# Optimization experiments

Hardware: AMD Instinct MI355X
Metric: run time of the kernel (lower is better)

The kernel has to match this reference:

```python
import jax, jax.numpy as jnp
import numpy as np

B, S, K, V = 2048, 128, 128, 128  # S == K == V required by the original code's matmul/broadcast
W_MAX = 1.0


def setup_inputs() -> dict:
    key = jax.random.key(0)
    ks = jax.random.split(key, 10)
    sc = 0.05
    return {
        "obs": jax.random.normal(ks[0], (B, S, K), jnp.float32),
        "brim_hidden": jax.random.normal(ks[1], (B, S, V), jnp.float32),
        "modulation": jax.random.uniform(ks[2], (B, S, 1), jnp.float32),
        "w_assoc": jax.random.normal(ks[3], (B, K, V), jnp.float32) * 0.1,
        "key_W": jax.random.normal(ks[4], (K, K), jnp.float32) * sc,
        "key_b": jnp.zeros((K,), jnp.float32),
        "val_W": jax.random.normal(ks[5], (V, V), jnp.float32) * sc,
        "val_b": jnp.zeros((V,), jnp.float32),
        "A_w": jax.random.normal(ks[6], (K, V), jnp.float32) * sc,
        "B_w": jax.random.normal(ks[7], (K, V), jnp.float32) * sc,
        "done_process_mdp": jnp.ones((B,), jnp.int32),
    }


def reference(obs, brim_hidden, modulation, w_assoc, key_W, key_b, val_W, val_b, A_w, B_w, done_process_mdp):
    # Encoders: single Linear each (key_encoder_layer = value_encoder_layer = 0)
    k = jnp.einsum("bsk,ok->bso", obs, key_W) + key_b            # [B,S,K]
    v = jnp.einsum("bsv,ov->bso", brim_hidden, val_W) + val_b    # [B,S,V]
    v = modulation * v                                           # neuromodulated values
    # Hebbian correlation and self-regularization terms
    corr = jnp.einsum("bsk,bsv->bkv", k, v)                      # key^T @ value  [B,K,V]
    reg = jnp.matmul(k, k)                                       # literal matmul(key, key); S==K -> [B,K,K]==[B,K,V]
    # Decay-scaled elementwise combine (A_w/B_w broadcast over batch)
    delta_w = A_w * (W_MAX - w_assoc) * corr - B_w * w_assoc * reg
    # Scatter update at done indices (mask form, equivalent since indices are unique)
    done = done_process_mdp.astype(bool)[:, None, None]
    return jnp.where(done, w_assoc + delta_w, w_assoc)
```

## Files before the change

### kernel.cpp

```cpp
#include <hip/hip_runtime.h>


typedef __attribute__((ext_vector_type(8))) short bf16x8;
typedef __attribute__((ext_vector_type(4))) float f32x4;

constexpr int D   = 128;
constexpr int LDB = 136;

__device__ __forceinline__ short f2bf(float x) {
    unsigned u = __builtin_bit_cast(unsigned, x);
    u += 0x7fff + ((u >> 16) & 1);
    return (short)(u >> 16);
}

__global__ void cvt_weights(const float* __restrict__ kw,
                            const float* __restrict__ vw,
                            short* __restrict__ o) {
    int i = blockIdx.x * 256 + threadIdx.x;
    o[i]         = f2bf(kw[i]);
    o[16384 + i] = f2bf(vw[i]);
}

__global__ __launch_bounds__(512, 1)
void hebb_mfma(const float* __restrict__ obs,
               const float* __restrict__ brim,
               const float* __restrict__ modu,
               const float* __restrict__ was,
               const short* __restrict__ keyWb,
               const float* __restrict__ keyB,
               const short* __restrict__ valWb,
               const float* __restrict__ valB,
               const float* __restrict__ Aw,
               const float* __restrict__ Bw,
               const int* __restrict__ done,
               float* __restrict__ out)
{
    __shared__ __align__(16) short xS [D * LDB];
    __shared__ __align__(16) short kS [D * LDB];
    __shared__ __align__(16) short kTS[D * LDB];
    __shared__ __align__(16) short vTS[D * LDB];

    const int b  = blockIdx.x;
    const int t  = threadIdx.x;
    const int w  = t >> 6;
    const int l  = t & 63;
    const int lr = l & 15;
    const int hg = l >> 4;

    {
        const float4* src = (const float4*)(obs + (size_t)b * D * D);
        #pragma unroll
        for (int i = 0; i < 8; ++i) {
            float4 g = src[i * 512 + t];
            int f = (i * 512 + t) * 4;
            int row = f >> 7, col = f & 127;
            short4 s4 = make_short4(f2bf(g.x), f2bf(g.y), f2bf(g.z), f2bf(g.w));
            *(short4*)&xS[row * LDB + col] = s4;
        }
    }
    __syncthreads();

    f32x4 acc[8], acc2[8];
    #pragma unroll
    for (int i = 0; i < 8; ++i) { acc[i] = f32x4{0.f,0.f,0.f,0.f}; acc2[i] = f32x4{0.f,0.f,0.f,0.f}; }

    for (int c = 0; c < 4; ++c) {
        const int c0 = c * 32 + 8 * hg;
        bf16x8 aK = *(const bf16x8*)&xS[(16 * w + lr) * LDB + c0];
        bf16x8 aT = *(const bf16x8*)&keyWb[(16 * w + lr) * D + c0];
        #pragma unroll
        for (int q = 0; q < 8; ++q) {
            bf16x8 bK = *(const bf16x8*)&keyWb[(16 * q + lr) * D + c0];
            bf16x8 bT = *(const bf16x8*)&xS[(16 * q + lr) * LDB + c0];
            acc[q]  = __builtin_amdgcn_mfma_f32_16x16x32_bf16(aK, bK, acc[q],  0, 0, 0);
            acc2[q] = __builtin_amdgcn_mfma_f32_16x16x32_bf16(aT, bT, acc2[q], 0, 0, 0);
        }
    }
    {
        float kbR[4];
        #pragma unroll
        for (int r = 0; r < 4; ++r) kbR[r] = keyB[16 * w + 4 * hg + r];
        #pragma unroll
        for (int q = 0; q < 8; ++q) {
            float kbC = keyB[16 * q + lr];
            #pragma unroll
            for (int r = 0; r < 4; ++r) {
                kS [(16 * w + 4 * hg + r) * LDB + 16 * q + lr] = f2bf(acc[q][r]  + kbC);
                kTS[(16 * w + 4 * hg + r) * LDB + 16 * q + lr] = f2bf(acc2[q][r] + kbR[r]);
            }
        }
    }
    __syncthreads();

    {
        const float4* src = (const float4*)(brim + (size_t)b * D * D);
        #pragma unroll
        for (int i = 0; i < 8; ++i) {
            float4 g = src[i * 512 + t];
            int f = (i * 512 + t) * 4;
            int row = f >> 7, col = f & 127;
            short4 s4 = make_short4(f2bf(g.x), f2bf(g.y), f2bf(g.z), f2bf(g.w));
            *(short4*)&xS[row * LDB + col] = s4;
        }
    }
    __syncthreads();

    #pragma unroll
    for (int i = 0; i < 8; ++i) acc[i] = f32x4{0.f,0.f,0.f,0.f};
    for (int c = 0; c < 4; ++c) {
        const int c0 = c * 32 + 8 * hg;
        bf16x8 aV = *(const bf16x8*)&valWb[(16 * w + lr) * D + c0];
        #pragma unroll
        for (int q = 0; q < 8; ++q) {
            bf16x8 bV = *(const bf16x8*)&xS[(16 * q + lr) * LDB + c0];
            acc[q] = __builtin_amdgcn_mfma_f32_16x16x32_bf16(aV, bV, acc[q], 0, 0, 0);
        }
    }
    {
        float vbR[4];
        #pragma unroll
        for (int r = 0; r < 4; ++r) vbR[r] = valB[16 * w + 4 * hg + r];
        #pragma unroll
        for (int q = 0; q < 8; ++q) {
            float m = modu[(size_t)b * D + 16 * q + lr];
            #pragma unroll
            for (int r = 0; r < 4; ++r)
                vTS[(16 * w + 4 * hg + r) * LDB + 16 * q + lr] = f2bf(m * (acc[q][r] + vbR[r]));
        }
    }
    __syncthreads();

    f32x4 cacc[8], racc[8];
    #pragma unroll
    for (int i = 0; i < 8; ++i) { cacc[i] = f32x4{0.f,0.f,0.f,0.f}; racc[i] = f32x4{0.f,0.f,0.f,0.f}; }

    for (int c = 0; c < 4; ++c) {
        const int c0 = c * 32 + 8 * hg;
        bf16x8 aC = *(const bf16x8*)&kTS[(16 * w + lr) * LDB + c0];
        bf16x8 aR = *(const bf16x8*)&kS [(16 * w + lr) * LDB + c0];
        #pragma unroll
        for (int q = 0; q < 8; ++q) {
            bf16x8 bC = *(const bf16x8*)&vTS[(16 * q + lr) * LDB + c0];
            bf16x8 bR = *(const bf16x8*)&kTS[(16 * q + lr) * LDB + c0];
            cacc[q] = __builtin_amdgcn_mfma_f32_16x16x32_bf16(aC, bC, cacc[q], 0, 0, 0);
            racc[q] = __builtin_amdgcn_mfma_f32_16x16x32_bf16(aR, bR, racc[q], 0, 0, 0);
        }
    }

    const float dsc = done[b] ? 1.0f : 0.0f;
    const size_t ob = (size_t)b * D * D;
    #pragma unroll
    for (int q = 0; q < 8; ++q) {
        const int j = 16 * q + lr;
        #pragma unroll
        for (int r = 0; r < 4; ++r) {
            const int i  = 16 * w + 4 * hg + r;
            const int ij = i * D + j;
            float wv = was[ob + ij];
            out[ob + ij] = wv + dsc * (Aw[ij] * (1.0f - wv) * cacc[q][r]
                                     - Bw[ij] * wv * racc[q][r]);
        }
    }
}

extern "C" void kernel_launch(void* const* d_in, const int* in_sizes, int n_in,
                              void* d_out, int out_size, void* d_ws, size_t ws_size,
                              hipStream_t stream) {
    const float* obs  = (const float*)d_in[0];
    const float* brim = (const float*)d_in[1];
    const float* modu = (const float*)d_in[2];
    const float* was  = (const float*)d_in[3];
    const float* keyW = (const float*)d_in[4];
    const float* keyB = (const float*)d_in[5];
    const float* valW = (const float*)d_in[6];
    const float* valB = (const float*)d_in[7];
    const float* Aw   = (const float*)d_in[8];
    const float* Bw   = (const float*)d_in[9];
    const int*   done = (const int*)d_in[10];
    float* out = (float*)d_out;

    const int B = in_sizes[10];
    short* wb = (short*)d_ws;

    hipLaunchKernelGGL(cvt_weights, dim3(64), dim3(256), 0, stream, keyW, valW, wb);
    hipLaunchKernelGGL(hebb_mfma, dim3(B), dim3(512), 0, stream,
                       obs, brim, modu, was, wb, keyB, wb + 16384, valB,
                       Aw, Bw, done, out);
}
```

Measured before the change: 494.9 us.

## Process eight batches per block with register prefetch and coalesced epilogue

Makes each workgroup loop over eight batch elements, so the grid is B/8 blocks. The next batch's obs and brim tiles and the current w_assoc tile are loaded into registers ahead of time, so global loads overlap with MFMA work. The epilogue stages corr and reg through LDS as bf16, which allows coalesced float4 reads of w_assoc, Aw and Bw and coalesced float4 writes of the output. Barriers become a lightweight lgkmcnt wait plus s_barrier. The costs are extra bf16 rounding of corr and reg, higher register pressure, and only 256 blocks, which may underfill the GPU.

```diff
diff --git a/kernel.cpp b/kernel.cpp
--- a/kernel.cpp
+++ b/kernel.cpp
@@ -6,12 +6,21 @@
 
 constexpr int D   = 128;
 constexpr int LDB = 136;
+constexpr int LDC = 132;
+constexpr int BPB = 8;
 
 __device__ __forceinline__ short f2bf(float x) {
     unsigned u = __builtin_bit_cast(unsigned, x);
     u += 0x7fff + ((u >> 16) & 1);
     return (short)(u >> 16);
 }
+__device__ __forceinline__ float bf2f(short s) {
+    unsigned u = ((unsigned)(unsigned short)s) << 16;
+    return __builtin_bit_cast(float, u);
+}
+
+#define LBAR() do { asm volatile("s_waitcnt lgkmcnt(0)" ::: "memory"); \
+                    __builtin_amdgcn_s_barrier(); } while (0)
 
 __global__ void cvt_weights(const float* __restrict__ kw,
                             const float* __restrict__ vw,
@@ -40,126 +49,168 @@
     __shared__ __align__(16) short kTS[D * LDB];
     __shared__ __align__(16) short vTS[D * LDB];
 
-    const int b  = blockIdx.x;
     const int t  = threadIdx.x;
     const int w  = t >> 6;
     const int l  = t & 63;
     const int lr = l & 15;
     const int hg = l >> 4;
-
+    const int b0 = blockIdx.x * BPB;
+
+    float kbR[4], vbR[4], kbC[8], vbC[8];
+    #pragma unroll
+    for (int r = 0; r < 4; ++r) { kbR[r] = keyB[16*w + 4*hg + r]; vbR[r] = valB[16*w + 4*hg + r]; }
+    #pragma unroll
+    for (int q = 0; q < 8; ++q) { kbC[q] = keyB[16*q + lr]; vbC[q] = valB[16*q + lr]; }
+    (void)vbC;
+
+    float4 obsR[8], brimR[8], wasR[8];
     {
-        const float4* src = (const float4*)(obs + (size_t)b * D * D);
+        const float4* os = (const float4*)(obs  + (size_t)b0 * D * D);
+        const float4* bs = (const float4*)(brim + (size_t)b0 * D * D);
+        #pragma unroll
+        for (int i = 0; i < 8; ++i) { obsR[i] = os[i*512 + t]; brimR[i] = bs[i*512 + t]; }
+    }
+    #pragma unroll
+    for (int i = 0; i < 8; ++i) {
+        int f = (i * 512 + t) * 4;
+        int row = f >> 7, col = f & 127;
+        *(short4*)&xS[row * LDB + col] =
+            make_short4(f2bf(obsR[i].x), f2bf(obsR[i].y), f2bf(obsR[i].z), f2bf(obsR[i].w));
+    }
+    LBAR();
+
+    for (int it = 0; it < BPB; ++it) {
+        const int b  = b0 + it;
+        const size_t ob = (size_t)b * D * D;
+
+        f32x4 acc[8], acc2[8];
+        #pragma unroll
+        for (int i = 0; i < 8; ++i) { acc[i] = f32x4{0.f,0.f,0.f,0.f}; acc2[i] = f32x4{0.f,0.f,0.f,0.f}; }
+
+        for (int c = 0; c < 4; ++c) {
+            const int c0 = c * 32 + 8 * hg;
+            bf16x8 aK = *(const bf16x8*)&xS[(16*w + lr) * LDB + c0];
+            bf16x8 aT = *(const bf16x8*)&keyWb[(16*w + lr) * D + c0];
+            #pragma unroll
+            for (int q = 0; q < 8; ++q) {
+                bf16x8 bK = *(const bf16x8*)&keyWb[(16*q + lr) * D + c0];
+                bf16x8 bT = *(const bf16x8*)&xS[(16*q + lr) * LDB + c0];
+                acc[q]  = __builtin_amdgcn_mfma_f32_16x16x32_bf16(aK, bK, acc[q],  0, 0, 0);
+                acc2[q] = __builtin_amdgcn_mfma_f32_16x16x32_bf16(aT, bT, acc2[q], 0, 0, 0);
+            }
+        }
+        #pragma unroll
+        for (int q = 0; q < 8; ++q) {
+            #pragma unroll
+            for (int r = 0; r < 4; ++r) {
+                kS [(16*w + 4*hg + r) * LDB + 16*q + lr] = f2bf(acc[q][r]  + kbC[q]);
+                kTS[(16*w + 4*hg + r) * LDB + 16*q + lr] = f2bf(acc2[q][r] + kbR[r]);
+            }
+        }
+        LBAR();
+
         #pragma unroll
         for (int i = 0; i < 8; ++i) {
-            float4 g = src[i * 512 + t];
             int f = (i * 512 + t) * 4;
             int row = f >> 7, col = f & 127;
-            short4 s4 = make_short4(f2bf(g.x), f2bf(g.y), f2bf(g.z), f2bf(g.w));
-            *(short4*)&xS[row * LDB + col] = s4;
-        }
-    }
-    __syncthreads();
-
-    f32x4 acc[8], acc2[8];
-    #pragma unroll
-    for (int i = 0; i < 8; ++i) { acc[i] = f32x4{0.f,0.f,0.f,0.f}; acc2[i] = f32x4{0.f,0.f,0.f,0.f}; }
-
-    for (int c = 0; c < 4; ++c) {
-        const int c0 = c * 32 + 8 * hg;
-        bf16x8 aK = *(const bf16x8*)&xS[(16 * w + lr) * LDB + c0];
-        bf16x8 aT = *(const bf16x8*)&keyWb[(16 * w + lr) * D + c0];
+            *(short4*)&xS[row * LDB + col] =
+                make_short4(f2bf(brimR[i].x), f2bf(brimR[i].y), f2bf(brimR[i].z), f2bf(brimR[i].w));
+        }
+        {
+            const float4* ws = (const float4*)(was + ob);
+            #pragma unroll
+            for (int ci = 0; ci < 8; ++ci) wasR[ci] = ws[ci*512 + t];
+        }
+        LBAR();
+
+        float mq[8];
+        #pragma unroll
+        for (int q = 0; q < 8; ++q) mq[q] = modu[(size_t)b * D + 16*q + lr];
+
+        f32x4 vacc[8];
+        #pragma unroll
+        for (int i = 0; i < 8; ++i) vacc[i] = f32x4{0.f,0.f,0.f,0.f};
+        for (int c = 0; c < 4; ++c) {
+            const int c0 = c * 32 + 8 * hg;
+            bf16x8 aV = *(const bf16x8*)&valWb[(16*w + lr) * D + c0];
+            #pragma unroll
+            for (int q = 0; q < 8; ++q) {
+                bf16x8 bV = *(const bf16x8*)&xS[(16*q + lr) * LDB + c0];
+                vacc[q] = __builtin_amdgcn_mfma_f32_16x16x32_bf16(aV, bV, vacc[q], 0, 0, 0);
+            }
+        }
         #pragma unroll
         for (int q = 0; q < 8; ++q) {
-            bf16x8 bK = *(const bf16x8*)&keyWb[(16 * q + lr) * D + c0];
-            bf16x8 bT = *(const bf16x8*)&xS[(16 * q + lr) * LDB + c0];
-            acc[q]  = __builtin_amdgcn_mfma_f32_16x16x32_bf16(aK, bK, acc[q],  0, 0, 0);
-            acc2[q] = __builtin_amdgcn_mfma_f32_16x16x32_bf16(aT, bT, acc2[q], 0, 0, 0);
-        }
-    }
-    {
-        float kbR[4];
-        #pragma unroll
-        for (int r = 0; r < 4; ++r) kbR[r] = keyB[16 * w + 4 * hg + r];
+            #pragma unroll
+            for (int r = 0; r < 4; ++r)
+                vTS[(16*w + 4*hg + r) * LDB + 16*q + lr] = f2bf(mq[q] * (vacc[q][r] + vbR[r]));
+        }
+        LBAR();
+
+        if (it < BPB - 1) {
+            const float4* os = (const float4*)(obs + (size_t)(b + 1) * D * D);
+            #pragma unroll
+            for (int i = 0; i < 8; ++i) obsR[i] = os[i*512 + t];
+        }
+        f32x4 cacc[8], racc[8];
+        #pragma unroll
+        for (int i = 0; i < 8; ++i) { cacc[i] = f32x4{0.f,0.f,0.f,0.f}; racc[i] = f32x4{0.f,0.f,0.f,0.f}; }
+
+        for (int c = 0; c < 4; ++c) {
+            const int c0 = c * 32 + 8 * hg;
+            bf16x8 aC = *(const bf16x8*)&kTS[(16*w + lr) * LDB + c0];
+            bf16x8 aR = *(const bf16x8*)&kS [(16*w + lr) * LDB + c0];
+            #pragma unroll
+            for (int q = 0; q < 8; ++q) {
+                bf16x8 bC = *(const bf16x8*)&vTS[(16*q + lr) * LDB + c0];
+                bf16x8 bR = *(const bf16x8*)&kTS[(16*q + lr) * LDB + c0];
+                cacc[q] = __builtin_amdgcn_mfma_f32_16x16x32_bf16(aC, bC, cacc[q], 0, 0, 0);
+                racc[q] = __builtin_amdgcn_mfma_f32_16x16x32_bf16(aR, bR, racc[q], 0, 0, 0);
+            }
+        }
+        LBAR();
+
         #pragma unroll
         for (int q = 0; q < 8; ++q) {
-            float kbC = keyB[16 * q + lr];
             #pragma unroll
             for (int r = 0; r < 4; ++r) {
-                kS [(16 * w + 4 * hg + r) * LDB + 16 * q + lr] = f2bf(acc[q][r]  + kbC);
-                kTS[(16 * w + 4 * hg + r) * LDB + 16 * q + lr] = f2bf(acc2[q][r] + kbR[r]);
-            }
-        }
-    }
-    __syncthreads();
-
-    {
-        const float4* src = (const float4*)(brim + (size_t)b * D * D);
-        #pragma unroll
-        for (int i = 0; i < 8; ++i) {
-            float4 g = src[i * 512 + t];
-            int f = (i * 512 + t) * 4;
-            int row = f >> 7, col = f & 127;
-            short4 s4 = make_short4(f2bf(g.x), f2bf(g.y), f2bf(g.z), f2bf(g.w));
-            *(short4*)&xS[row * LDB + col] = s4;
-        }
-    }
-    __syncthreads();
-
-    #pragma unroll
-    for (int i = 0; i < 8; ++i) acc[i] = f32x4{0.f,0.f,0.f,0.f};
-    for (int c = 0; c < 4; ++c) {
-        const int c0 = c * 32 + 8 * hg;
-        bf16x8 aV = *(const bf16x8*)&valWb[(16 * w + lr) * D + c0];
-        #pragma unroll
-        for (int q = 0; q < 8; ++q) {
-            bf16x8 bV = *(const bf16x8*)&xS[(16 * q + lr) * LDB + c0];
-            acc[q] = __builtin_amdgcn_mfma_f32_16x16x32_bf16(aV, bV, acc[q], 0, 0, 0);
-        }
-    }
-    {
-        float vbR[4];
-        #pragma unroll
-        for (int r = 0; r < 4; ++r) vbR[r] = valB[16 * w + 4 * hg + r];
-        #pragma unroll
-        for (int q = 0; q < 8; ++q) {
-            float m = modu[(size_t)b * D + 16 * q + lr];
-            #pragma unroll
-            for (int r = 0; r < 4; ++r)
-                vTS[(16 * w + 4 * hg + r) * LDB + 16 * q + lr] = f2bf(m * (acc[q][r] + vbR[r]));
-        }
-    }
-    __syncthreads();
-
-    f32x4 cacc[8], racc[8];
-    #pragma unroll
-    for (int i = 0; i < 8; ++i) { cacc[i] = f32x4{0.f,0.f,0.f,0.f}; racc[i] = f32x4{0.f,0.f,0.f,0.f}; }
-
-    for (int c = 0; c < 4; ++c) {
-        const int c0 = c * 32 + 8 * hg;
-        bf16x8 aC = *(const bf16x8*)&kTS[(16 * w + lr) * LDB + c0];
-        bf16x8 aR = *(const bf16x8*)&kS [(16 * w + lr) * LDB + c0];
-        #pragma unroll
-        for (int q = 0; q < 8; ++q) {
-            bf16x8 bC = *(const bf16x8*)&vTS[(16 * q + lr) * LDB + c0];
-            bf16x8 bR = *(const bf16x8*)&kTS[(16 * q + lr) * LDB + c0];
-            cacc[q] = __builtin_amdgcn_mfma_f32_16x16x32_bf16(aC, bC, cacc[q], 0, 0, 0);
-            racc[q] = __builtin_amdgcn_mfma_f32_16x16x32_bf16(aR, bR, racc[q], 0, 0, 0);
-        }
-    }
-
-    const float dsc = done[b] ? 1.0f : 0.0f;
-    const size_t ob = (size_t)b * D * D;
-    #pragma unroll
-    for (int q = 0; q < 8; ++q) {
-        const int j = 16 * q + lr;
-        #pragma unroll
-        for (int r = 0; r < 4; ++r) {
-            const int i  = 16 * w + 4 * hg + r;
-            const int ij = i * D + j;
-            float wv = was[ob + ij];
-            out[ob + ij] = wv + dsc * (Aw[ij] * (1.0f - wv) * cacc[q][r]
-                                     - Bw[ij] * wv * racc[q][r]);
-        }
+                kS [(16*w + 4*hg + r) * LDC + 16*q + lr] = f2bf(cacc[q][r]);
+                kTS[(16*w + 4*hg + r) * LDC + 16*q + lr] = f2bf(racc[q][r]);
+            }
+        }
+        LBAR();
+
+        const float dsc = done[b] ? 1.0f : 0.0f;
+        #pragma unroll
+        for (int ci = 0; ci < 8; ++ci) {
+            const int row = 16*ci + (t >> 5);
+            const int j0  = (t & 31) * 4;
+            short4 cs = *(const short4*)&kS [row * LDC + j0];
+            short4 rs = *(const short4*)&kTS[row * LDC + j0];
+            float4 w4 = wasR[ci];
+            float4 a4 = *(const float4*)&Aw[row * D + j0];
+            float4 b4 = *(const float4*)&Bw[row * D + j0];
+            float4 o;
+            o.x = w4.x + dsc * (a4.x * (1.f - w4.x) * bf2f(cs.x) - b4.x * w4.x * bf2f(rs.x));
+            o.y = w4.y + dsc * (a4.y * (1.f - w4.y) * bf2f(cs.y) - b4.y * w4.y * bf2f(rs.y));
+            o.z = w4.z + dsc * (a4.z * (1.f - w4.z) * bf2f(cs.z) - b4.z * w4.z * bf2f(rs.z));
+            o.w = w4.w + dsc * (a4.w * (1.f - w4.w) * bf2f(cs.w) - b4.w * w4.w * bf2f(rs.w));
+            *(float4*)&out[ob + row * D + j0] = o;
+        }
+
+        if (it < BPB - 1) {
+            #pragma unroll
+            for (int i = 0; i < 8; ++i) {
+                int f = (i * 512 + t) * 4;
+                int row = f >> 7, col = f & 127;
+                *(short4*)&xS[row * LDB + col] =
+                    make_short4(f2bf(obsR[i].x), f2bf(obsR[i].y), f2bf(obsR[i].z), f2bf(obsR[i].w));
+            }
+            const float4* bs = (const float4*)(brim + (size_t)(b + 1) * D * D);
+            #pragma unroll
+            for (int i = 0; i < 8; ++i) brimR[i] = bs[i*512 + t];
+        }
+        LBAR();
     }
 }
 
@@ -183,7 +234,7 @@
     short* wb = (short*)d_ws;
 
     hipLaunchKernelGGL(cvt_weights, dim3(64), dim3(256), 0, stream, keyW, valW, wb);
-    hipLaunchKernelGGL(hebb_mfma, dim3(B), dim3(512), 0, stream,
+    hipLaunchKernelGGL(hebb_mfma, dim3(B / BPB), dim3(512), 0, stream,
                        obs, brim, modu, was, wb, keyB, wb + 16384, valB,
                        Aw, Bw, done, out);
 }
```

Result: slower. 736.5 us (+48.8%).
